# Performance work log

Hardware: AMD Instinct MI355X
Metric: run time of the kernel (lower is better)

Reference implementation:

```python
import jax, jax.numpy as jnp
import numpy as np

FEAT_DIM = 128
GUIDE_DIM = 128
NIR_DIM = 32
H_LR, W_LR = 128, 128
H_HR, W_HR = 256, 256
IMNET_IN = FEAT_DIM + 2 * GUIDE_DIM + 2  # 386


def make_coord_1d(n):
    # pixel-center coords in [-1, 1]: (2i+1)/n - 1
    return (2.0 * jnp.arange(n, dtype=jnp.float32) + 1.0) / n - 1.0


def nearest_sample(img, cy, cx):
    """F.grid_sample(img, grid, mode='nearest', align_corners=False, padding='zeros').
    img: [b, C, h, w]; cy, cx: [N] normalized coords (cy -> h axis, cx -> w axis).
    Returns sampled values [b, C, N] and the pixel-center coords (qcy, qcx) the
    nearest sample corresponds to (0 when out of range, matching zero padding)."""
    h, w = img.shape[-2], img.shape[-1]
    iy = jnp.round(((cy + 1.0) * h - 1.0) * 0.5).astype(jnp.int32)  # round-half-even == nearbyint
    ix = jnp.round(((cx + 1.0) * w - 1.0) * 0.5).astype(jnp.int32)
    valid = (iy >= 0) & (iy < h) & (ix >= 0) & (ix < w)
    iyc = jnp.clip(iy, 0, h - 1)
    ixc = jnp.clip(ix, 0, w - 1)
    out = img[:, :, iyc, ixc]                       # [b, C, N] gather
    out = jnp.where(valid[None, None, :], out, 0.0)
    qcy = jnp.where(valid, (2.0 * iyc.astype(jnp.float32) + 1.0) / h - 1.0, 0.0)
    qcx = jnp.where(valid, (2.0 * ixc.astype(jnp.float32) + 1.0) / w - 1.0, 0.0)
    return out, qcy, qcx


def mlp(x, W1, b1, W2, b2, W3, b3):
    x = jax.nn.relu(x @ W1 + b1)
    x = jax.nn.relu(x @ W2 + b2)
    return x @ W3 + b3


def setup_inputs() -> dict:
    key = jax.random.key(0)
    ks = jax.random.split(key, 9)
    return {
        "feat": jax.random.normal(ks[0], (1, FEAT_DIM, H_LR, W_LR), jnp.float32),
        "lr_guide": jax.random.normal(ks[1], (1, GUIDE_DIM, H_LR, W_LR), jnp.float32),
        "hr_guide": jax.random.normal(ks[2], (1, GUIDE_DIM, H_HR, W_HR), jnp.float32),
        "W1": jax.random.normal(ks[3], (IMNET_IN, 256), jnp.float32) * 0.05,
        "b1": jax.random.normal(ks[4], (256,), jnp.float32) * 0.05,
        "W2": jax.random.normal(ks[5], (256, 128), jnp.float32) * 0.05,
        "b2": jax.random.normal(ks[6], (128,), jnp.float32) * 0.05,
        "W3": jax.random.normal(ks[7], (128, NIR_DIM), jnp.float32) * 0.05,
        "b3": jax.random.normal(ks[8], (NIR_DIM,), jnp.float32) * 0.05,
    }


def reference(feat, lr_guide, hr_guide, W1, b1, W2, b2, W3, b3):
    b, _, h, w = feat.shape
    _, cg, H, W = hr_guide.shape
    N = H * W
    featc = jnp.concatenate([lr_guide, feat], axis=1)        # [b, guide+feat, h, w]

    gy, gx = jnp.meshgrid(make_coord_1d(H), make_coord_1d(W), indexing="ij")
    cy = gy.reshape(-1)                                      # [N] coord[:, 0] (h axis)
    cx = gx.reshape(-1)                                      # [N] coord[:, 1] (w axis)

    q_guide_hr = hr_guide.reshape(b, cg, N).transpose(0, 2, 1)  # [b, N, cg]

    # feat_ : gather at the unshifted coord (identical across neighbors)
    feat_b, _, _ = nearest_sample(featc, cy, cx)
    feat_b = feat_b.transpose(0, 2, 1)                       # [b, N, C]

    rx = 1.0 / h
    ry = 1.0 / w
    preds, gcs = [], []
    for vx in (-1.0, 1.0):
        for vy in (-1.0, 1.0):
            q_feat, qcy, qcx = nearest_sample(featc, cy + vx * rx, cx + vy * ry)
            q_feat = q_feat.transpose(0, 2, 1)               # [b, N, C]
            rel = jnp.stack([(cy - qcy) * h, (cx - qcx) * w], axis=-1)  # [N, 2]
            rel = jnp.broadcast_to(rel[None], (b, N, 2))
            inp = jnp.concatenate([q_feat, q_guide_hr, rel], axis=-1)  # [b, N, 386]
            preds.append(mlp(inp, W1, b1, W2, b2, W3, b3))   # [b, N, NIR]
            # bilateral color weight: dot over channels [-4:-1]
            gcs.append(jnp.sum(feat_b[..., -4:-1] * q_feat[..., -4:-1], axis=-1))
    preds = jnp.stack(preds, axis=-1)                        # [b, N, NIR, 4]
    weight = jax.nn.softmax(jnp.stack(gcs, axis=-1), axis=-1)  # [b, N, 4]
    ret = jnp.sum(preds * weight[:, :, None, :], axis=-1)    # [b, N, NIR]
    return ret.transpose(0, 2, 1).reshape(b, -1, H, W)
```

## Files before the change

### kernel.cpp

```cpp
#include <hip/hip_runtime.h>
#include <hip/hip_bf16.h>


using bf16x8 = __attribute__((ext_vector_type(8))) __bf16;
using f32x4  = __attribute__((ext_vector_type(4))) float;

__device__ __forceinline__ float bf2f(unsigned short u){
  unsigned int x = ((unsigned int)u) << 16;
  return __builtin_bit_cast(float, x);
}
__device__ __forceinline__ unsigned short f2bf(float f){
  unsigned int x = __builtin_bit_cast(unsigned int, f);
  unsigned int r = x + 0x7fffu + ((x >> 16) & 1u);
  return (unsigned short)(r >> 16);
}
__device__ __forceinline__ bf16x8 ld8(const ushort* p){
  uint4 r = *(const uint4*)p;
  return __builtin_bit_cast(bf16x8, r);
}

struct RowMeta { int spos; float relY, relX; };
__device__ __forceinline__ RowMeta row_meta(int Y, int X, int br){
  int ivx = br >> 1, ivy = br & 1;
  int validY, iy; float relY;
  if (ivx == 0){ validY = (Y >= 1);   iy = (Y-1) >> 1; relY = (Y & 1) ?  0.5f :  1.5f; }
  else         { validY = (Y <= 254); iy = (Y+1) >> 1; relY = (Y & 1) ? -1.5f : -0.5f; }
  int validX, ix; float relX;
  if (ivy == 0){ validX = (X >= 1);   ix = (X-1) >> 1; relX = (X & 1) ?  0.5f :  1.5f; }
  else         { validX = (X <= 254); ix = (X+1) >> 1; relX = (X & 1) ? -1.5f : -0.5f; }
  RowMeta r;
  if (validY && validX){ r.spos = iy*128 + ix; r.relY = relY; r.relX = relX; }
  else { r.spos = -1; r.relY = (float)Y + 0.5f - 128.0f; r.relX = (float)X + 0.5f - 128.0f; }
  return r;
}

__global__ __launch_bounds__(256) void convert_weights(
    const float* __restrict__ W1, const float* __restrict__ W2,
    const float* __restrict__ W3,
    ushort* __restrict__ W1t,
    ushort* __restrict__ W2t,
    ushort* __restrict__ W3t)
{
  int i = blockIdx.x*256 + threadIdx.x;
  { int k = i >> 8, n = i & 255; W1t[n*384 + k] = f2bf(W1[i]); }
  if (i < 32768){ int k = i >> 7, n = i & 127; W2t[n*256 + k] = f2bf(W2[i]); }
  if (i < 4096) { int k = i >> 5, n = i & 31;  W3t[n*128 + k] = f2bf(W3[i]); }
}

__global__ __launch_bounds__(256) void stage1_gemm(
    const float* __restrict__ src0, const float* __restrict__ src1, int M,
    const ushort* __restrict__ Bt, int koff,
    const float* __restrict__ bias,
    ushort* __restrict__ outp)
{
  __shared__ ushort A[64*136];
  const int t = threadIdx.x;
  const int w = t >> 6, lane = t & 63, quad = lane >> 4, l15 = lane & 15;
  const int pos0 = blockIdx.x * 64;
  const int nhalf = src1 ? 2 : 1;

  f32x4 acc[4][4];
  #pragma unroll
  for (int mt=0; mt<4; mt++)
    #pragma unroll
    for (int nt=0; nt<4; nt++) acc[mt][nt] = f32x4{0.f,0.f,0.f,0.f};

  for (int h=0; h<nhalf; h++){
    const float* src = h ? src1 : src0;
    #pragma unroll
    for (int i=0; i<32; i++){
      int f = i*256 + t;
      int k = f >> 6, mm = f & 63;
      A[mm*136 + k] = f2bf(src[(size_t)k*M + pos0 + mm]);
    }
    __syncthreads();
    bf16x8 b[4][4];
    #pragma unroll
    for (int kt=0; kt<4; kt++)
      #pragma unroll
      for (int nt=0; nt<4; nt++)
        b[kt][nt] = ld8(&Bt[(size_t)(w*64 + nt*16 + l15)*384 + koff + h*128 + kt*32 + quad*8]);
    #pragma unroll
    for (int mt=0; mt<4; mt++)
      #pragma unroll
      for (int kt=0; kt<4; kt++){
        bf16x8 a = ld8(&A[(mt*16 + l15)*136 + kt*32 + quad*8]);
        #pragma unroll
        for (int nt=0; nt<4; nt++)
          acc[mt][nt] = __builtin_amdgcn_mfma_f32_16x16x32_bf16(a, b[kt][nt], acc[mt][nt], 0,0,0);
      }
    __syncthreads();
  }
  #pragma unroll
  for (int mt=0; mt<4; mt++)
    #pragma unroll
    for (int nt=0; nt<4; nt++){
      int n = w*64 + nt*16 + l15;
      float bv = bias ? bias[n] : 0.0f;
      #pragma unroll
      for (int r=0; r<4; r++){
        int mm = mt*16 + quad*4 + r;
        outp[(size_t)(pos0 + mm)*256 + n] = f2bf(acc[mt][nt][r] + bv);
      }
    }
}

__global__ __launch_bounds__(256, 3) void main_fused(
    const float* __restrict__ feat,
    const float* __restrict__ hr_guide,
    const float* __restrict__ W1,
    const float* __restrict__ b1v,
    const float* __restrict__ b2v,
    const float* __restrict__ b3v,
    const ushort* __restrict__ U,
    const ushort* __restrict__ W1t,
    const ushort* __restrict__ W2t,
    const ushort* __restrict__ W3t,
    float* __restrict__ outp)
{
  __shared__ __align__(16) ushort A1[64*264];
  __shared__ __align__(16) ushort Gt[16*264];
  __shared__ __align__(16) float  w1r[2][256];
  __shared__ float gcs[64];
  __shared__ float wgt[64];

  const int t = threadIdx.x;
  const int w = t >> 6, lane = t & 63, quad = lane >> 4, l15 = lane & 15;
  const int Y  = blockIdx.x >> 4;
  const int X0 = (blockIdx.x & 15) << 4;

  const int m   = t >> 2;
  const int pix = m >> 2, br = m & 3;
  const int c0  = (t & 3) * 64;
  RowMeta rm = row_meta(Y, X0 + pix, br);

  uint4 uu[8];
  if (rm.spos >= 0){
    const ushort* Up = U + (size_t)rm.spos*256 + c0;
    #pragma unroll
    for (int j=0; j<8; j++) uu[j] = *(const uint4*)(Up + j*8);
  } else {
    #pragma unroll
    for (int j=0; j<8; j++) uu[j] = make_uint4(0u,0u,0u,0u);
  }

  {
    ushort* Ahr = A1;
    #pragma unroll
    for (int i=0; i<2; i++){
      int id = i*256 + t;
      int ch = id >> 2, xq = id & 3;
      float4 v = *(const float4*)(hr_guide + (size_t)ch*65536 + Y*256 + X0 + xq*4);
      Ahr[(xq*4+0)*136 + ch] = f2bf(v.x);
      Ahr[(xq*4+1)*136 + ch] = f2bf(v.y);
      Ahr[(xq*4+2)*136 + ch] = f2bf(v.z);
      Ahr[(xq*4+3)*136 + ch] = f2bf(v.w);
    }
  }
  w1r[0][t] = W1[384*256 + t];
  w1r[1][t] = W1[385*256 + t];

  if (t < 64){
    RowMeta g = row_meta(Y, X0 + (t>>2), t & 3);
    float gc = 0.0f;
    if (g.spos >= 0){
      int bpos = (Y>>1)*128 + ((X0 + (t>>2)) >> 1);
      #pragma unroll
      for (int cc=0; cc<3; cc++)
        gc += feat[(size_t)(124+cc)*16384 + bpos] * feat[(size_t)(124+cc)*16384 + g.spos];
    }
    gcs[t] = gc;
  }
  __syncthreads();

  if (t < 16){
    float g0 = gcs[t*4+0], g1 = gcs[t*4+1], g2 = gcs[t*4+2], g3 = gcs[t*4+3];
    float mx = fmaxf(fmaxf(g0,g1), fmaxf(g2,g3));
    float e0 = __expf(g0-mx), e1 = __expf(g1-mx), e2 = __expf(g2-mx), e3 = __expf(g3-mx);
    float inv = 1.0f/(e0+e1+e2+e3);
    wgt[t*4+0]=e0*inv; wgt[t*4+1]=e1*inv; wgt[t*4+2]=e2*inv; wgt[t*4+3]=e3*inv;
  }
  {
    f32x4 accg[4];
    #pragma unroll
    for (int nt=0; nt<4; nt++) accg[nt] = f32x4{0.f,0.f,0.f,0.f};
    #pragma unroll
    for (int kt=0; kt<4; kt++){
      bf16x8 a = ld8(&A1[l15*136 + kt*32 + quad*8]);
      #pragma unroll
      for (int nt=0; nt<4; nt++){
        bf16x8 b = ld8(&W1t[(size_t)(w*64 + nt*16 + l15)*384 + 256 + kt*32 + quad*8]);
        accg[nt] = __builtin_amdgcn_mfma_f32_16x16x32_bf16(a, b, accg[nt], 0,0,0);
      }
    }
    #pragma unroll
    for (int nt=0; nt<4; nt++){
      int n = w*64 + nt*16 + l15;
      float bv = b1v[n];
      #pragma unroll
      for (int r=0; r<4; r++)
        Gt[(quad*4+r)*264 + n] = f2bf(accg[nt][r] + bv);
    }
  }
  __syncthreads();

  bf16x8 b2f[8][2];
  #pragma unroll
  for (int kt=0; kt<8; kt++)
    #pragma unroll
    for (int nt=0; nt<2; nt++)
      b2f[kt][nt] = ld8(&W2t[(size_t)(w*32 + nt*16 + l15)*256 + kt*32 + quad*8]);

  {
    float relY = rm.relY, relX = rm.relX;
    #pragma unroll
    for (int jj=0; jj<8; jj++){
      int c = c0 + jj*8;
      union { uint4 v; ushort s[8]; } gu, uv, ov;
      gu.v = *(const uint4*)&Gt[pix*264 + c];
      uv.v = uu[jj];
      float r0[8], r1[8];
      *(float4*)&r0[0] = *(const float4*)&w1r[0][c];
      *(float4*)&r0[4] = *(const float4*)&w1r[0][c+4];
      *(float4*)&r1[0] = *(const float4*)&w1r[1][c];
      *(float4*)&r1[4] = *(const float4*)&w1r[1][c+4];
      #pragma unroll
      for (int i=0; i<8; i++){
        float h = bf2f(uv.s[i]) + bf2f(gu.s[i]) + relY*r0[i] + relX*r1[i];
        ov.s[i] = f2bf(fmaxf(h, 0.0f));
      }
      *(uint4*)&A1[m*264 + c] = ov.v;
    }
  }
  __syncthreads();

  f32x4 acc2[4][2];
  #pragma unroll
  for (int mt=0; mt<4; mt++)
    #pragma unroll
    for (int nt=0; nt<2; nt++) acc2[mt][nt] = f32x4{0.f,0.f,0.f,0.f};
  #pragma unroll
  for (int mt=0; mt<4; mt++)
    #pragma unroll
    for (int kt=0; kt<8; kt++){
      bf16x8 a = ld8(&A1[(mt*16 + l15)*264 + kt*32 + quad*8]);
      #pragma unroll
      for (int nt=0; nt<2; nt++)
        acc2[mt][nt] = __builtin_amdgcn_mfma_f32_16x16x32_bf16(a, b2f[kt][nt], acc2[mt][nt], 0,0,0);
    }
  __syncthreads();

  bf16x8 b3f[4][2];
  #pragma unroll
  for (int kt=0; kt<4; kt++)
    #pragma unroll
    for (int nt=0; nt<2; nt++)
      b3f[kt][nt] = ld8(&W3t[(size_t)(nt*16 + l15)*128 + kt*32 + quad*8]);

  {
    ushort* A2 = A1;
    float bias0 = b2v[w*32 + l15], bias1 = b2v[w*32 + 16 + l15];
    #pragma unroll
    for (int mt=0; mt<4; mt++)
      #pragma unroll
      for (int nt=0; nt<2; nt++){
        int n = w*32 + nt*16 + l15;
        float bv = nt ? bias1 : bias0;
        #pragma unroll
        for (int r=0; r<4; r++){
          int mm = mt*16 + quad*4 + r;
          A2[mm*136 + n] = f2bf(fmaxf(acc2[mt][nt][r] + bv, 0.0f));
        }
      }
  }
  __syncthreads();

  {
    const ushort* A2 = A1;
    f32x4 acc3[2] = { f32x4{0.f,0.f,0.f,0.f}, f32x4{0.f,0.f,0.f,0.f} };
    #pragma unroll
    for (int kt=0; kt<4; kt++){
      bf16x8 a = ld8(&A2[(w*16 + l15)*136 + kt*32 + quad*8]);
      #pragma unroll
      for (int nt=0; nt<2; nt++)
        acc3[nt] = __builtin_amdgcn_mfma_f32_16x16x32_bf16(a, b3f[kt][nt], acc3[nt], 0,0,0);
    }
    int lp = w*4 + quad;
    int X = X0 + lp;
    float w0 = wgt[lp*4+0], w1 = wgt[lp*4+1], w2 = wgt[lp*4+2], w3 = wgt[lp*4+3];
    #pragma unroll
    for (int nt=0; nt<2; nt++){
      int n = nt*16 + l15;
      float bb = b3v[n];
      float v = w0*(acc3[nt][0]+bb) + w1*(acc3[nt][1]+bb)
              + w2*(acc3[nt][2]+bb) + w3*(acc3[nt][3]+bb);
      outp[(size_t)n*65536 + (size_t)Y*256 + X] = v;
    }
  }
}

extern "C" void kernel_launch(void* const* d_in, const int* in_sizes, int n_in,
                              void* d_out, int out_size, void* d_ws, size_t ws_size,
                              hipStream_t stream)
{
  const float* feat     = (const float*)d_in[0];
  const float* lr_guide = (const float*)d_in[1];
  const float* hr_guide = (const float*)d_in[2];
  const float* W1       = (const float*)d_in[3];
  const float* b1       = (const float*)d_in[4];
  const float* W2       = (const float*)d_in[5];
  const float* b2       = (const float*)d_in[6];
  const float* W3       = (const float*)d_in[7];
  const float* b3       = (const float*)d_in[8];
  float* outp = (float*)d_out;

  char* ws = (char*)d_ws;
  ushort* W1t = (ushort*)(ws);
  ushort* W2t = (ushort*)(ws + 196608);
  ushort* W3t = (ushort*)(ws + 196608 + 65536);
  ushort* Ub  = (ushort*)(ws + 196608 + 65536 + 8192);

  convert_weights<<<384, 256, 0, stream>>>(W1, W2, W3, W1t, W2t, W3t);
  stage1_gemm<<<256, 256, 0, stream>>>(lr_guide, feat, 16384, W1t, 0, nullptr, Ub);
  main_fused<<<4096, 256, 0, stream>>>(feat, hr_guide, W1, b1, b2, b3,
                                       Ub, W1t, W2t, W3t, outp);
}
```

Baseline: 202.1 us.

## Split U GEMM into transpose-prep and smaller GEMM; widen main kernel to 512 threads

The weight-conversion kernel now also transposes lr_guide and feat into a bf16 position-major buffer. A separate small-tile GEMM then computes U from that buffer over 1024 blocks instead of 256. The main fused kernel runs with 512 threads per block. It uses XOR-swizzled unpadded LDS layouts in place of padding, packed bf16 conversion via v_cvt_pk_bf16_f32, and loads W2 fragments per k-step instead of holding them all in registers. These changes aim to raise parallelism and occupancy and cut LDS bank conflicts, at the cost of an extra kernel launch and an 8MB intermediate round trip through memory.

```diff
diff --git a/kernel.cpp b/kernel.cpp
--- a/kernel.cpp
+++ b/kernel.cpp
@@ -14,9 +14,24 @@
   unsigned int r = x + 0x7fffu + ((x >> 16) & 1u);
   return (unsigned short)(r >> 16);
 }
+__device__ __forceinline__ unsigned int cvt_pk_bf16(float lo, float hi){
+  unsigned int r;
+  asm("v_cvt_pk_bf16_f32 %0, %1, %2" : "=v"(r) : "v"(lo), "v"(hi));
+  return r;
+}
 __device__ __forceinline__ bf16x8 ld8(const ushort* p){
   uint4 r = *(const uint4*)p;
   return __builtin_bit_cast(bf16x8, r);
+}
+
+__device__ __forceinline__ int swz256i(int row, int c){
+  return row*256 + ((c & ~0x38) | ((((c>>3) + (c>>6) + 2*row) & 7) << 3));
+}
+__device__ __forceinline__ int swz128i(int row, int c){
+  return row*128 + ((c & ~0x38) | ((((c>>3) + (c>>6) + 2*row) & 7) << 3));
+}
+__device__ __forceinline__ int swzT(int row, int c){
+  return row*256 + ((c & ~0x38) | ((((c>>3) + (c>>6) + row) & 7) << 3));
 }
 
 struct RowMeta { int spos; float relY, relX; };
@@ -34,78 +49,79 @@
   return r;
 }
 
-__global__ __launch_bounds__(256) void convert_weights(
+__global__ __launch_bounds__(256) void prep(
     const float* __restrict__ W1, const float* __restrict__ W2,
     const float* __restrict__ W3,
+    const float* __restrict__ lr_guide, const float* __restrict__ feat,
     ushort* __restrict__ W1t,
     ushort* __restrict__ W2t,
-    ushort* __restrict__ W3t)
+    ushort* __restrict__ W3t,
+    ushort* __restrict__ Ft)
 {
-  int i = blockIdx.x*256 + threadIdx.x;
-  { int k = i >> 8, n = i & 255; W1t[n*384 + k] = f2bf(W1[i]); }
-  if (i < 32768){ int k = i >> 7, n = i & 127; W2t[n*256 + k] = f2bf(W2[i]); }
-  if (i < 4096) { int k = i >> 5, n = i & 31;  W3t[n*128 + k] = f2bf(W3[i]); }
-}
-
-__global__ __launch_bounds__(256) void stage1_gemm(
-    const float* __restrict__ src0, const float* __restrict__ src1, int M,
-    const ushort* __restrict__ Bt, int koff,
-    const float* __restrict__ bias,
-    ushort* __restrict__ outp)
+  __shared__ ushort T[32*256];
+  const int b = blockIdx.x, t = threadIdx.x;
+  if (b < 512){
+    const int pos0 = b*32;
+    #pragma unroll
+    for (int i=0;i<32;i++){
+      int k = i*8 + (t>>5), pos = t & 31;
+      const float* src = (k < 128) ? lr_guide : feat;
+      T[swzT(pos, k)] = f2bf(src[(size_t)(k & 127)*16384 + pos0 + pos]);
+    }
+    __syncthreads();
+    const int pos = t>>3, ul = t&7;
+    #pragma unroll
+    for (int jj=0;jj<4;jj++){
+      int c = ul*32 + jj*8;
+      union { uint4 v; ushort s[8]; } x;
+      x.v = *(const uint4*)&T[swzT(pos, c)];
+      *(uint4*)&Ft[(size_t)(pos0+pos)*256 + c] = x.v;
+    }
+  } else {
+    int i = (b-512)*256 + t;
+    { int k = i >> 8, n = i & 255; W1t[n*384 + k] = f2bf(W1[i]); }
+    if (i < 32768){ int k = i >> 7, n = i & 127; W2t[n*256 + k] = f2bf(W2[i]); }
+    if (i < 4096) { int k = i >> 5, n = i & 31;  W3t[n*128 + k] = f2bf(W3[i]); }
+  }
+}
+
+__global__ __launch_bounds__(256) void u_gemm(
+    const ushort* __restrict__ Ft, const ushort* __restrict__ W1t,
+    ushort* __restrict__ U)
 {
-  __shared__ ushort A[64*136];
   const int t = threadIdx.x;
   const int w = t >> 6, lane = t & 63, quad = lane >> 4, l15 = lane & 15;
-  const int pos0 = blockIdx.x * 64;
-  const int nhalf = src1 ? 2 : 1;
-
-  f32x4 acc[4][4];
-  #pragma unroll
-  for (int mt=0; mt<4; mt++)
-    #pragma unroll
-    for (int nt=0; nt<4; nt++) acc[mt][nt] = f32x4{0.f,0.f,0.f,0.f};
-
-  for (int h=0; h<nhalf; h++){
-    const float* src = h ? src1 : src0;
-    #pragma unroll
-    for (int i=0; i<32; i++){
-      int f = i*256 + t;
-      int k = f >> 6, mm = f & 63;
-      A[mm*136 + k] = f2bf(src[(size_t)k*M + pos0 + mm]);
-    }
-    __syncthreads();
-    bf16x8 b[4][4];
-    #pragma unroll
-    for (int kt=0; kt<4; kt++)
-      #pragma unroll
-      for (int nt=0; nt<4; nt++)
-        b[kt][nt] = ld8(&Bt[(size_t)(w*64 + nt*16 + l15)*384 + koff + h*128 + kt*32 + quad*8]);
-    #pragma unroll
-    for (int mt=0; mt<4; mt++)
-      #pragma unroll
-      for (int kt=0; kt<4; kt++){
-        bf16x8 a = ld8(&A[(mt*16 + l15)*136 + kt*32 + quad*8]);
-        #pragma unroll
-        for (int nt=0; nt<4; nt++)
-          acc[mt][nt] = __builtin_amdgcn_mfma_f32_16x16x32_bf16(a, b[kt][nt], acc[mt][nt], 0,0,0);
-      }
-    __syncthreads();
-  }
-  #pragma unroll
-  for (int mt=0; mt<4; mt++)
-    #pragma unroll
-    for (int nt=0; nt<4; nt++){
-      int n = w*64 + nt*16 + l15;
-      float bv = bias ? bias[n] : 0.0f;
-      #pragma unroll
-      for (int r=0; r<4; r++){
-        int mm = mt*16 + quad*4 + r;
-        outp[(size_t)(pos0 + mm)*256 + n] = f2bf(acc[mt][nt][r] + bv);
-      }
-    }
-}
-
-__global__ __launch_bounds__(256, 3) void main_fused(
+  const int pos0 = (blockIdx.x >> 1) * 32;
+  const int nh   = blockIdx.x & 1;
+
+  f32x4 acc[2][2];
+  #pragma unroll
+  for (int a=0;a<2;a++) { acc[a][0] = f32x4{0.f,0.f,0.f,0.f}; acc[a][1] = f32x4{0.f,0.f,0.f,0.f}; }
+
+  #pragma unroll
+  for (int kt=0; kt<8; kt++){
+    const int ko = kt*32 + quad*8;
+    bf16x8 a0 = ld8(&Ft[(size_t)(pos0 +      l15)*256 + ko]);
+    bf16x8 a1 = ld8(&Ft[(size_t)(pos0 + 16 + l15)*256 + ko]);
+    bf16x8 b0 = ld8(&W1t[(size_t)(nh*128 + w*32 +      l15)*384 + ko]);
+    bf16x8 b1 = ld8(&W1t[(size_t)(nh*128 + w*32 + 16 + l15)*384 + ko]);
+    acc[0][0] = __builtin_amdgcn_mfma_f32_16x16x32_bf16(a0, b0, acc[0][0], 0,0,0);
+    acc[0][1] = __builtin_amdgcn_mfma_f32_16x16x32_bf16(a0, b1, acc[0][1], 0,0,0);
+    acc[1][0] = __builtin_amdgcn_mfma_f32_16x16x32_bf16(a1, b0, acc[1][0], 0,0,0);
+    acc[1][1] = __builtin_amdgcn_mfma_f32_16x16x32_bf16(a1, b1, acc[1][1], 0,0,0);
+  }
+  #pragma unroll
+  for (int mt=0; mt<2; mt++)
+    #pragma unroll
+    for (int nt=0; nt<2; nt++){
+      int n = nh*128 + w*32 + nt*16 + l15;
+      #pragma unroll
+      for (int r=0; r<4; r++)
+        U[(size_t)(pos0 + mt*16 + quad*4 + r)*256 + n] = f2bf(acc[mt][nt][r]);
+    }
+}
+
+__global__ __launch_bounds__(512, 6) void main_fused(
     const float* __restrict__ feat,
     const float* __restrict__ hr_guide,
     const float* __restrict__ W1,
@@ -118,8 +134,8 @@
     const ushort* __restrict__ W3t,
     float* __restrict__ outp)
 {
-  __shared__ __align__(16) ushort A1[64*264];
-  __shared__ __align__(16) ushort Gt[16*264];
+  __shared__ __align__(16) ushort A1[64*256];
+  __shared__ __align__(16) ushort Gt[16*256];
   __shared__ __align__(16) float  w1r[2][256];
   __shared__ float gcs[64];
   __shared__ float wgt[64];
@@ -129,36 +145,30 @@
   const int Y  = blockIdx.x >> 4;
   const int X0 = (blockIdx.x & 15) << 4;
 
-  const int m   = t >> 2;
+  const int m   = t >> 3;
+  const int ul  = t & 7;
   const int pix = m >> 2, br = m & 3;
-  const int c0  = (t & 3) * 64;
   RowMeta rm = row_meta(Y, X0 + pix, br);
 
-  uint4 uu[8];
+  uint4 uu[4];
   if (rm.spos >= 0){
-    const ushort* Up = U + (size_t)rm.spos*256 + c0;
-    #pragma unroll
-    for (int j=0; j<8; j++) uu[j] = *(const uint4*)(Up + j*8);
+    const ushort* Up = U + (size_t)rm.spos*256 + ul*32;
+    #pragma unroll
+    for (int j=0; j<4; j++) uu[j] = *(const uint4*)(Up + j*8);
   } else {
     #pragma unroll
-    for (int j=0; j<8; j++) uu[j] = make_uint4(0u,0u,0u,0u);
-  }
-
-  {
-    ushort* Ahr = A1;
-    #pragma unroll
-    for (int i=0; i<2; i++){
-      int id = i*256 + t;
-      int ch = id >> 2, xq = id & 3;
-      float4 v = *(const float4*)(hr_guide + (size_t)ch*65536 + Y*256 + X0 + xq*4);
-      Ahr[(xq*4+0)*136 + ch] = f2bf(v.x);
-      Ahr[(xq*4+1)*136 + ch] = f2bf(v.y);
-      Ahr[(xq*4+2)*136 + ch] = f2bf(v.z);
-      Ahr[(xq*4+3)*136 + ch] = f2bf(v.w);
-    }
-  }
-  w1r[0][t] = W1[384*256 + t];
-  w1r[1][t] = W1[385*256 + t];
+    for (int j=0; j<4; j++) uu[j] = make_uint4(0u,0u,0u,0u);
+  }
+
+  {
+    int ch = t >> 2, xq = t & 3;
+    float4 v = *(const float4*)(hr_guide + (size_t)ch*65536 + Y*256 + X0 + xq*4);
+    A1[swz256i(xq*4+0, ch)] = f2bf(v.x);
+    A1[swz256i(xq*4+1, ch)] = f2bf(v.y);
+    A1[swz256i(xq*4+2, ch)] = f2bf(v.z);
+    A1[swz256i(xq*4+3, ch)] = f2bf(v.w);
+  }
+  w1r[t>>8][t&255] = W1[(size_t)(384 + (t>>8))*256 + (t&255)];
 
   if (t < 64){
     RowMeta g = row_meta(Y, X0 + (t>>2), t & 3);
@@ -181,121 +191,96 @@
     wgt[t*4+0]=e0*inv; wgt[t*4+1]=e1*inv; wgt[t*4+2]=e2*inv; wgt[t*4+3]=e3*inv;
   }
   {
-    f32x4 accg[4];
-    #pragma unroll
-    for (int nt=0; nt<4; nt++) accg[nt] = f32x4{0.f,0.f,0.f,0.f};
+    f32x4 accg[2] = { f32x4{0.f,0.f,0.f,0.f}, f32x4{0.f,0.f,0.f,0.f} };
     #pragma unroll
     for (int kt=0; kt<4; kt++){
-      bf16x8 a = ld8(&A1[l15*136 + kt*32 + quad*8]);
-      #pragma unroll
-      for (int nt=0; nt<4; nt++){
-        bf16x8 b = ld8(&W1t[(size_t)(w*64 + nt*16 + l15)*384 + 256 + kt*32 + quad*8]);
+      bf16x8 a = ld8(&A1[swz256i(l15, kt*32 + quad*8)]);
+      #pragma unroll
+      for (int nt=0; nt<2; nt++){
+        bf16x8 b = ld8(&W1t[(size_t)(w*32 + nt*16 + l15)*384 + 256 + kt*32 + quad*8]);
         accg[nt] = __builtin_amdgcn_mfma_f32_16x16x32_bf16(a, b, accg[nt], 0,0,0);
       }
     }
     #pragma unroll
-    for (int nt=0; nt<4; nt++){
-      int n = w*64 + nt*16 + l15;
+    for (int nt=0; nt<2; nt++){
+      int n = w*32 + nt*16 + l15;
       float bv = b1v[n];
       #pragma unroll
       for (int r=0; r<4; r++)
-        Gt[(quad*4+r)*264 + n] = f2bf(accg[nt][r] + bv);
-    }
-  }
-  __syncthreads();
-
-  bf16x8 b2f[8][2];
-  #pragma unroll
-  for (int kt=0; kt<8; kt++)
-    #pragma unroll
-    for (int nt=0; nt<2; nt++)
-      b2f[kt][nt] = ld8(&W2t[(size_t)(w*32 + nt*16 + l15)*256 + kt*32 + quad*8]);
-
-  {
-    float relY = rm.relY, relX = rm.relX;
-    #pragma unroll
-    for (int jj=0; jj<8; jj++){
-      int c = c0 + jj*8;
-      union { uint4 v; ushort s[8]; } gu, uv, ov;
-      gu.v = *(const uint4*)&Gt[pix*264 + c];
+        Gt[swz256i(quad*4+r, n)] = f2bf(accg[nt][r] + bv);
+    }
+  }
+  __syncthreads();
+
+  {
+    const float relY = rm.relY, relX = rm.relX;
+    #pragma unroll
+    for (int jj=0; jj<4; jj++){
+      const int c = ul*32 + jj*8;
+      union { uint4 v; ushort s[8]; } gu, uv;
+      gu.v = *(const uint4*)&Gt[swz256i(pix, c)];
       uv.v = uu[jj];
       float r0[8], r1[8];
       *(float4*)&r0[0] = *(const float4*)&w1r[0][c];
       *(float4*)&r0[4] = *(const float4*)&w1r[0][c+4];
       *(float4*)&r1[0] = *(const float4*)&w1r[1][c];
       *(float4*)&r1[4] = *(const float4*)&w1r[1][c+4];
-      #pragma unroll
-      for (int i=0; i<8; i++){
-        float h = bf2f(uv.s[i]) + bf2f(gu.s[i]) + relY*r0[i] + relX*r1[i];
-        ov.s[i] = f2bf(fmaxf(h, 0.0f));
+      unsigned int ov[4];
+      #pragma unroll
+      for (int i=0; i<4; i++){
+        float h0 = bf2f(uv.s[2*i+0]) + bf2f(gu.s[2*i+0]) + relY*r0[2*i+0] + relX*r1[2*i+0];
+        float h1 = bf2f(uv.s[2*i+1]) + bf2f(gu.s[2*i+1]) + relY*r0[2*i+1] + relX*r1[2*i+1];
+        ov[i] = cvt_pk_bf16(fmaxf(h0, 0.0f), fmaxf(h1, 0.0f));
       }
-      *(uint4*)&A1[m*264 + c] = ov.v;
-    }
-  }
-  __syncthreads();
-
-  f32x4 acc2[4][2];
-  #pragma unroll
-  for (int mt=0; mt<4; mt++)
-    #pragma unroll
-    for (int nt=0; nt<2; nt++) acc2[mt][nt] = f32x4{0.f,0.f,0.f,0.f};
-  #pragma unroll
-  for (int mt=0; mt<4; mt++)
-    #pragma unroll
-    for (int kt=0; kt<8; kt++){
-      bf16x8 a = ld8(&A1[(mt*16 + l15)*264 + kt*32 + quad*8]);
-      #pragma unroll
-      for (int nt=0; nt<2; nt++)
-        acc2[mt][nt] = __builtin_amdgcn_mfma_f32_16x16x32_bf16(a, b2f[kt][nt], acc2[mt][nt], 0,0,0);
-    }
-  __syncthreads();
-
-  bf16x8 b3f[4][2];
+      *(uint4*)&A1[swz256i(m, c)] = make_uint4(ov[0],ov[1],ov[2],ov[3]);
+    }
+  }
+  __syncthreads();
+
+  const int mt = w >> 1, nh = w & 1;
+  f32x4 acc2[4];
+  #pragma unroll
+  for (int nt=0; nt<4; nt++) acc2[nt] = f32x4{0.f,0.f,0.f,0.f};
+  #pragma unroll
+  for (int kt=0; kt<8; kt++){
+    bf16x8 a = ld8(&A1[swz256i(mt*16 + l15, kt*32 + quad*8)]);
+    #pragma unroll
+    for (int nt=0; nt<4; nt++){
+      bf16x8 b = ld8(&W2t[(size_t)(nh*64 + nt*16 + l15)*256 + kt*32 + quad*8]);
+      acc2[nt] = __builtin_amdgcn_mfma_f32_16x16x32_bf16(a, b, acc2[nt], 0,0,0);
+    }
+  }
+  __syncthreads();
+
+  bf16x8 b3f[4];
   #pragma unroll
   for (int kt=0; kt<4; kt++)
-    #pragma unroll
-    for (int nt=0; nt<2; nt++)
-      b3f[kt][nt] = ld8(&W3t[(size_t)(nt*16 + l15)*128 + kt*32 + quad*8]);
-
-  {
-    ushort* A2 = A1;
-    float bias0 = b2v[w*32 + l15], bias1 = b2v[w*32 + 16 + l15];
-    #pragma unroll
-    for (int mt=0; mt<4; mt++)
-      #pragma unroll
-      for (int nt=0; nt<2; nt++){
-        int n = w*32 + nt*16 + l15;
-        float bv = nt ? bias1 : bias0;
-        #pragma unroll
-        for (int r=0; r<4; r++){
-          int mm = mt*16 + quad*4 + r;
-          A2[mm*136 + n] = f2bf(fmaxf(acc2[mt][nt][r] + bv, 0.0f));
-        }
-      }
-  }
-  __syncthreads();
-
-  {
-    const ushort* A2 = A1;
-    f32x4 acc3[2] = { f32x4{0.f,0.f,0.f,0.f}, f32x4{0.f,0.f,0.f,0.f} };
+    b3f[kt] = ld8(&W3t[(size_t)(nh*16 + l15)*128 + kt*32 + quad*8]);
+  {
+    #pragma unroll
+    for (int nt=0; nt<4; nt++){
+      int n = nh*64 + nt*16 + l15;
+      float bv = b2v[n];
+      #pragma unroll
+      for (int r=0; r<4; r++)
+        A1[swz128i(mt*16 + quad*4 + r, n)] = f2bf(fmaxf(acc2[nt][r] + bv, 0.0f));
+    }
+  }
+  __syncthreads();
+
+  {
+    f32x4 acc3 = f32x4{0.f,0.f,0.f,0.f};
     #pragma unroll
     for (int kt=0; kt<4; kt++){
-      bf16x8 a = ld8(&A2[(w*16 + l15)*136 + kt*32 + quad*8]);
-      #pragma unroll
-      for (int nt=0; nt<2; nt++)
-        acc3[nt] = __builtin_amdgcn_mfma_f32_16x16x32_bf16(a, b3f[kt][nt], acc3[nt], 0,0,0);
-    }
-    int lp = w*4 + quad;
-    int X = X0 + lp;
-    float w0 = wgt[lp*4+0], w1 = wgt[lp*4+1], w2 = wgt[lp*4+2], w3 = wgt[lp*4+3];
-    #pragma unroll
-    for (int nt=0; nt<2; nt++){
-      int n = nt*16 + l15;
-      float bb = b3v[n];
-      float v = w0*(acc3[nt][0]+bb) + w1*(acc3[nt][1]+bb)
-              + w2*(acc3[nt][2]+bb) + w3*(acc3[nt][3]+bb);
-      outp[(size_t)n*65536 + (size_t)Y*256 + X] = v;
-    }
+      bf16x8 a = ld8(&A1[swz128i(mt*16 + l15, kt*32 + quad*8)]);
+      acc3 = __builtin_amdgcn_mfma_f32_16x16x32_bf16(a, b3f[kt], acc3, 0,0,0);
+    }
+    int lp = mt*4 + quad;
+    int n  = nh*16 + l15;
+    float bb = b3v[n];
+    float v = wgt[lp*4+0]*(acc3[0]+bb) + wgt[lp*4+1]*(acc3[1]+bb)
+            + wgt[lp*4+2]*(acc3[2]+bb) + wgt[lp*4+3]*(acc3[3]+bb);
+    outp[(size_t)n*65536 + (size_t)Y*256 + X0 + lp] = v;
   }
 }
 
@@ -317,11 +302,12 @@
   char* ws = (char*)d_ws;
   ushort* W1t = (ushort*)(ws);
   ushort* W2t = (ushort*)(ws + 196608);
-  ushort* W3t = (ushort*)(ws + 196608 + 65536);
-  ushort* Ub  = (ushort*)(ws + 196608 + 65536 + 8192);
-
-  convert_weights<<<384, 256, 0, stream>>>(W1, W2, W3, W1t, W2t, W3t);
-  stage1_gemm<<<256, 256, 0, stream>>>(lr_guide, feat, 16384, W1t, 0, nullptr, Ub);
-  main_fused<<<4096, 256, 0, stream>>>(feat, hr_guide, W1, b1, b2, b3,
+  ushort* W3t = (ushort*)(ws + 262144);
+  ushort* Ft  = (ushort*)(ws + 270336);
+  ushort* Ub  = (ushort*)(ws + 270336 + 8388608);
+
+  prep<<<896, 256, 0, stream>>>(W1, W2, W3, lr_guide, feat, W1t, W2t, W3t, Ft);
+  u_gemm<<<1024, 256, 0, stream>>>(Ft, W1t, Ub);
+  main_fused<<<4096, 512, 0, stream>>>(feat, hr_guide, W1, b1, b2, b3,
                                        Ub, W1t, W2t, W3t, outp);
 }
```

Measured after the change: 285.8 us. 41.4% more time.
